# Kernel tuning notes

Measured on AMD Instinct MI355X. Metric: run time of the kernel, lower is better.

The kernel has to match this reference:

```python
import jax, jax.numpy as jnp
import numpy as np

# 3x3 window roll offsets, row-major as in PatchShift2D.shift_content
SHIFTS = [(1, 1), (1, 0), (1, -1), (0, 1), (0, 0), (0, -1), (-1, 1), (-1, 0), (-1, -1)]
NUM_WIN = 9


def patch_shift(x, inv):
    # x: [B, T, H, W, C]; pad C up to multiple of 9 and H,W by 1, roll each
    # of the 9 channel groups by a distinct (h, w) offset, then crop back.
    B, T, H, W, C = x.shape
    Ch = int(np.ceil(C / NUM_WIN) * NUM_WIN)
    xp = jnp.pad(x, ((0, 0), (0, 0), (1, 1), (1, 1), (0, Ch - C)))
    m = -1 if inv else 1
    parts = jnp.split(xp, NUM_WIN, axis=-1)
    shifted = [jnp.roll(p, (m * sh, m * sw), axis=(2, 3))
               for p, (sh, sw) in zip(parts, SHIFTS)]
    return jnp.concatenate(shifted, axis=-1)[:, :, 1:H + 1, 1:W + 1, :C]


def _gelu(v):
    return jax.nn.gelu(v, approximate=False)  # torch nn.GELU default (erf)


def setup_inputs() -> dict:
    key = jax.random.key(0)
    ks = jax.random.split(key, 14)
    B, T, H, W, C = 2, 8, 56, 56, 512
    HID = 1024
    s = 0.02
    return {
        "x": jax.random.normal(ks[0], (B, T, H, W, C), dtype=jnp.float32),
        "fc_w": s * jax.random.normal(ks[1], (C, HID), dtype=jnp.float32),
        "fc_b": jnp.zeros((HID,), jnp.float32),
        "fc1_w": s * jax.random.normal(ks[2], (HID, C), dtype=jnp.float32),
        "fc1_b": jnp.zeros((C,), jnp.float32),
        "fc2_w": s * jax.random.normal(ks[3], (HID, C), dtype=jnp.float32),
        "fc2_b": jnp.zeros((C,), jnp.float32),
        "rw1_w": s * jax.random.normal(ks[4], (C, C // 4), dtype=jnp.float32),
        "rw1_b": jnp.zeros((C // 4,), jnp.float32),
        "rw2_w": s * jax.random.normal(ks[5], (C // 4, 2 * C), dtype=jnp.float32),
        "rw2_b": jnp.zeros((2 * C,), jnp.float32),
        "proj_w": s * jax.random.normal(ks[6], (C, C), dtype=jnp.float32),
        "proj_b": jnp.zeros((C,), jnp.float32),
    }


def reference(x, fc_w, fc_b, fc1_w, fc1_b, fc2_w, fc2_b,
              rw1_w, rw1_b, rw2_w, rw2_b, proj_w, proj_b):
    B, T, H, W, C = x.shape
    xh = _gelu(x @ fc_w + fc_b)                                  # [B,T,H,W,HID]
    h = patch_shift(_gelu(patch_shift(xh, False) @ fc1_w + fc1_b), True)  # [B,T,H,W,C]
    w = _gelu(xh @ fc2_w + fc2_b)                                 # [B,T,H,W,C]
    a = (h + w).mean(axis=(1, 2, 3))                              # [B,C]
    a = _gelu(a @ rw1_w + rw1_b) @ rw2_w + rw2_b                  # [B,2C]
    a = jax.nn.softmax(a.reshape(B, C, 2).transpose(2, 0, 1), axis=0)  # [2,B,C]
    a = a[:, :, None, None, None, :]                              # [2,B,1,1,1,C]
    out = h * a[0] + w * a[1]
    return out @ proj_w + proj_b
```

## Files before the change

### kernel.cpp

```cpp
#include <hip/hip_runtime.h>
#include <hip/hip_bf16.h>
#include <stdint.h>


typedef __attribute__((ext_vector_type(8))) short short8;
typedef __attribute__((ext_vector_type(4))) float floatx4;
typedef unsigned int uint;
typedef unsigned short ushort;

#define NTOK   50176
#define HWIMG  3136

__device__ __forceinline__ float gelu_exact(float v) {
    return 0.5f * v * (1.0f + erff(v * 0.70710678118654752440f));
}
__device__ __forceinline__ float gelu_fast(float v) {
    float u = v * (0.7978845608f + 0.0356774081f * v * v);
    return v * __builtin_amdgcn_rcpf(1.0f + __expf(-2.0f * u));
}

__device__ __forceinline__ int shift_h(int g) { return 1 - g / 3; }
__device__ __forceinline__ int shift_w(int g) { return 1 - g % 3; }

typedef const __attribute__((address_space(1))) uint* gas_ptr;
typedef __attribute__((address_space(3))) uint* las_ptr;

__device__ __forceinline__ void async_copy16(const void* g, void* l) {
    gas_ptr gp = (gas_ptr)(uintptr_t)g;
    las_ptr lp = (las_ptr)(uint32_t)(uintptr_t)l;
    __builtin_amdgcn_global_load_lds(gp, lp, 16, 0, 0);
}

template <int EPI, bool SHIFTA>
__global__ __launch_bounds__(256) void gemm_bt(
    const __hip_bfloat16* __restrict__ A,
    const __hip_bfloat16* __restrict__ Bt,
    const float* __restrict__ bias,
    void* __restrict__ Cout,
    float* __restrict__ ssum, int N, int K)
{
    constexpr int NBUF = SHIFTA ? 1 : 2;
    __shared__ __align__(16) __hip_bfloat16 As[NBUF * 128 * 32];
    __shared__ __align__(16) __hip_bfloat16 Bs[NBUF * 128 * 32];

    const int t    = threadIdx.x;
    const int lane = t & 63;
    const int wave = t >> 6;
    const int wm   = wave >> 1;
    const int wn   = wave & 1;

    const int nbn  = gridDim.x;
    const int flat = blockIdx.y * nbn + blockIdx.x;
    const int xcd  = flat & 7;
    const int j    = flat >> 3;
    const int jd   = j / nbn;
    const int bm   = xcd * 49 + jd;
    const int bn   = j - jd * nbn;

    const int ar0 = bm * 128 + (t >> 2);
    const int ar1 = ar0 + 64;
    const int ac  = (t & 3) * 8;

    const __hip_bfloat16* ga0 = A  + (size_t)ar0 * K + ac;
    const __hip_bfloat16* ga1 = ga0 + (size_t)64 * K;
    const __hip_bfloat16* gb0 = Bt + (size_t)(bn * 128 + (t >> 2)) * K + ac;
    const __hip_bfloat16* gb1 = gb0 + (size_t)64 * K;

    floatx4 acc[4][4] = {};

    const int kq = (lane >> 4) * 8;
    const int ml = lane & 15;

    if constexpr (!SHIFTA) {
        auto stage = [&](int buf) {
            __hip_bfloat16* lA = &As[buf * 4096 + t * 8];
            __hip_bfloat16* lB = &Bs[buf * 4096 + t * 8];
            async_copy16(ga0, lA);
            async_copy16(ga1, lA + 2048);
            async_copy16(gb0, lB);
            async_copy16(gb1, lB + 2048);
            ga0 += 32; ga1 += 32; gb0 += 32; gb1 += 32;
        };

        const int nt = K >> 5;
        stage(0);
        for (int tt = 0; tt < nt; ++tt) {
            const int cur = tt & 1;
            if (tt + 1 < nt) {
                stage(cur ^ 1);
                asm volatile("s_waitcnt vmcnt(4)" ::: "memory");
            } else {
                asm volatile("s_waitcnt vmcnt(0)" ::: "memory");
            }
            __builtin_amdgcn_s_barrier();
            asm volatile("" ::: "memory");

            const int ab = cur * 4096;
            short8 af[4], bf[4];
#pragma unroll
            for (int i = 0; i < 4; i++) {
                af[i] = *(const short8*)&As[ab + (wm * 64 + i * 16 + ml) * 32 + kq];
                bf[i] = *(const short8*)&Bs[ab + (wn * 64 + i * 16 + ml) * 32 + kq];
            }
#pragma unroll
            for (int mi = 0; mi < 4; mi++)
#pragma unroll
                for (int ni = 0; ni < 4; ni++)
                    acc[mi][ni] = __builtin_amdgcn_mfma_f32_16x16x32_bf16(
                        af[mi], bf[ni], acc[mi][ni], 0, 0, 0);

            asm volatile("" ::: "memory");
            __builtin_amdgcn_s_barrier();
        }
    } else {
        __hip_bfloat16* la0 = &As[t * 8];
        __hip_bfloat16* la1 = &As[t * 8 + 2048];
        __hip_bfloat16* lb0 = &Bs[t * 8];
        __hip_bfloat16* lb1 = &Bs[t * 8 + 2048];

        const int rem0 = ar0 % HWIMG, rem1 = ar1 % HWIMG;
        const int oh0 = rem0 / 56, ow0 = rem0 - oh0 * 56;
        const int oh1 = rem1 / 56, ow1 = rem1 - oh1 * 56;

        for (int k0 = 0; k0 < K; k0 += 32) {
            async_copy16(gb0, lb0);
            async_copy16(gb1, lb1);
            gb0 += 32; gb1 += 32;

            uint4 av0 = {0, 0, 0, 0}, av1 = {0, 0, 0, 0};
            {
                const int c0 = k0 + ac;
                const int g  = c0 / 114;
                const int ge = (c0 + 7) / 114;
                if (g == ge) {
                    const int sh = shift_h(g), sw = shift_w(g);
                    const int off = sh * 56 + sw;
                    if ((unsigned)(oh0 - sh) < 56u && (unsigned)(ow0 - sw) < 56u)
                        av0 = *(const uint4*)(A + (size_t)(ar0 - off) * K + c0);
                    if ((unsigned)(oh1 - sh) < 56u && (unsigned)(ow1 - sw) < 56u)
                        av1 = *(const uint4*)(A + (size_t)(ar1 - off) * K + c0);
                } else {
                    union { ushort us[8]; uint4 v; } p0, p1;
#pragma unroll
                    for (int e = 0; e < 8; e++) {
                        const int c  = c0 + e;
                        const int gg = c / 114;
                        const int sh = shift_h(gg), sw = shift_w(gg);
                        const int off = sh * 56 + sw;
                        ushort v0 = 0, v1 = 0;
                        if ((unsigned)(oh0 - sh) < 56u && (unsigned)(ow0 - sw) < 56u)
                            v0 = *(const ushort*)(A + (size_t)(ar0 - off) * K + c);
                        if ((unsigned)(oh1 - sh) < 56u && (unsigned)(ow1 - sw) < 56u)
                            v1 = *(const ushort*)(A + (size_t)(ar1 - off) * K + c);
                        p0.us[e] = v0; p1.us[e] = v1;
                    }
                    av0 = p0.v; av1 = p1.v;
                }
            }

            asm volatile("s_waitcnt vmcnt(0)" ::: "memory");
            *(uint4*)la0 = av0;
            *(uint4*)la1 = av1;
            __syncthreads();

            short8 af[4], bf[4];
#pragma unroll
            for (int i = 0; i < 4; i++) {
                af[i] = *(const short8*)&As[(wm * 64 + i * 16 + ml) * 32 + kq];
                bf[i] = *(const short8*)&Bs[(wn * 64 + i * 16 + ml) * 32 + kq];
            }
#pragma unroll
            for (int mi = 0; mi < 4; mi++)
#pragma unroll
                for (int ni = 0; ni < 4; ni++)
                    acc[mi][ni] = __builtin_amdgcn_mfma_f32_16x16x32_bf16(
                        af[mi], bf[ni], acc[mi][ni], 0, 0, 0);
            __syncthreads();
        }
    }

    const int rq = (lane >> 4) * 4;

    int cols[4], gsh[4], gsw[4];
    float bv[4];
    float sum[4] = {0.f, 0.f, 0.f, 0.f};
#pragma unroll
    for (int ni = 0; ni < 4; ni++) {
        const int col = bn * 128 + wn * 64 + ni * 16 + ml;
        cols[ni] = col;
        bv[ni] = bias[col];
        if (EPI == 2) { const int g = col / 57; gsh[ni] = shift_h(g); gsw[ni] = shift_w(g); }
    }

#pragma unroll
    for (int mi = 0; mi < 4; mi++) {
        const int row0 = bm * 128 + wm * 64 + mi * 16 + rq;
        int phr[4], pwr[4];
        if (EPI == 2) {
            const int bt_ = row0 / HWIMG;
            const int rem = row0 - bt_ * HWIMG;
            const int ph0 = rem / 56;
            const int pw0 = rem - ph0 * 56;
#pragma unroll
            for (int r = 0; r < 4; r++) {
                int pw = pw0 + r, ph = ph0;
                if (pw >= 56) { pw -= 56; ph += 1; }
                if (ph >= 56) { ph = 0; }
                phr[r] = ph; pwr[r] = pw;
            }
        }
#pragma unroll
        for (int ni = 0; ni < 4; ni++) {
            const int col = cols[ni];
#pragma unroll
            for (int r = 0; r < 4; r++) {
                const int tok = row0 + r;
                float v = acc[mi][ni][r] + bv[ni];
                if (EPI != 0) v = gelu_fast(v);
                if (EPI == 0) {
                    ((float*)Cout)[(size_t)tok * N + col] = v;
                } else if (EPI == 1) {
                    ((__hip_bfloat16*)Cout)[(size_t)tok * N + col] = __float2bfloat16(v);
                } else if (EPI == 2) {
                    const int th = phr[r] - gsh[ni], tw = pwr[r] - gsw[ni];
                    if ((unsigned)th < 56u && (unsigned)tw < 56u) {
                        ((__hip_bfloat16*)Cout)[(size_t)(tok - gsh[ni] * 56 - gsw[ni]) * N + col]
                            = __float2bfloat16(v);
                        sum[ni] += v;
                    }
                } else {
                    ((__hip_bfloat16*)Cout)[(size_t)tok * N + col] = __float2bfloat16(v);
                    sum[ni] += v;
                }
            }
        }
    }

    if (EPI == 2 || EPI == 3) {
        const int b = (bm >= 196) ? 1 : 0;
#pragma unroll
        for (int ni = 0; ni < 4; ni++) {
            float s = sum[ni];
            s += __shfl_xor(s, 16, 64);
            s += __shfl_xor(s, 32, 64);
            if (lane < 16) atomicAdd(&ssum[b * 512 + cols[ni]], s);
        }
    }
}

template <int C, int GS, int SGN>
__global__ __launch_bounds__(256) void zero_holes(__hip_bfloat16* __restrict__ buf)
{
    const int i = blockIdx.x * 256 + threadIdx.x;
    const int c = i % C;
    const int p = i / C;
    const int bt = p / 220, fp = p % 220;
    int oh, ow;
    if (fp < 56)       { oh = 0;        ow = fp; }
    else if (fp < 112) { oh = 55;       ow = fp - 56; }
    else if (fp < 166) { oh = fp - 111; ow = 0; }
    else               { oh = fp - 165; ow = 55; }
    const int g = c / GS;
    const int ih = oh - SGN * shift_h(g);
    const int iw = ow - SGN * shift_w(g);
    if ((unsigned)ih >= 56u || (unsigned)iw >= 56u)
        buf[((size_t)(bt * HWIMG + oh * 56 + ow)) * C + c] = __float2bfloat16(0.0f);
}

__global__ __launch_bounds__(256) void cvt_x(const float4* __restrict__ x,
                                             __hip_bfloat16* __restrict__ xb)
{
    int i = blockIdx.x * 256 + threadIdx.x;
    float4 v = x[i];
    __hip_bfloat16 b0 = __float2bfloat16(v.x);
    __hip_bfloat16 b1 = __float2bfloat16(v.y);
    __hip_bfloat16 b2 = __float2bfloat16(v.z);
    __hip_bfloat16 b3 = __float2bfloat16(v.w);
    uint2 o;
    o.x = (uint)*(ushort*)&b0 | ((uint)*(ushort*)&b1 << 16);
    o.y = (uint)*(ushort*)&b2 | ((uint)*(ushort*)&b3 << 16);
    *(uint2*)&xb[(size_t)i * 4] = o;
}

__global__ __launch_bounds__(256) void prep_w(
    const float* __restrict__ fcw,  const float* __restrict__ fc1w,
    const float* __restrict__ fc2w, const float* __restrict__ projw,
    __hip_bfloat16* __restrict__ fcwT, __hip_bfloat16* __restrict__ fc1T,
    __hip_bfloat16* __restrict__ fc2T, __hip_bfloat16* __restrict__ projT)
{
    int i = blockIdx.x * 256 + threadIdx.x;
    if (i < 524288) {
        int n = i >> 9, k = i & 511;
        fcwT[i] = __float2bfloat16(fcw[k * 1024 + n]);
    } else if (i < 1048576) {
        int j = i - 524288;
        int n = j >> 10, k = j & 1023;
        fc1T[j] = __float2bfloat16(fc1w[k * 512 + n]);
    } else if (i < 1572864) {
        int j = i - 1048576;
        int n = j >> 10, k = j & 1023;
        fc2T[j] = __float2bfloat16(fc2w[k * 512 + n]);
    } else if (i < 1835008) {
        int j = i - 1572864;
        int n = j >> 9, k = j & 511;
        projT[j] = __float2bfloat16(projw[k * 512 + n]);
    }
}

__global__ __launch_bounds__(256) void tiny_mlp(
    const float* __restrict__ s0, const float* __restrict__ s1,
    const float* __restrict__ rw1_w, const float* __restrict__ rw1_b,
    const float* __restrict__ rw2_w, const float* __restrict__ rw2_b,
    float* __restrict__ a0, float* __restrict__ a1)
{
    __shared__ float mean[1024];
    __shared__ float z[256];
    __shared__ float av[2048];
    const int t = threadIdx.x;
    for (int i = t; i < 1024; i += 256)
        mean[i] = (s0[i] + s1[i]) * (1.0f / 25088.0f);
    __syncthreads();
    {
        const int b = t >> 7, j = t & 127;
        float acc = rw1_b[j];
        for (int cc = 0; cc < 512; cc++)
            acc += mean[b * 512 + cc] * rw1_w[cc * 128 + j];
        z[t] = gelu_exact(acc);
    }
    __syncthreads();
    for (int i = t; i < 2048; i += 256) {
        const int b = i >> 10, o = i & 1023;
        float acc = rw2_b[o];
        for (int j = 0; j < 128; j++)
            acc += z[b * 128 + j] * rw2_w[j * 1024 + o];
        av[i] = acc;
    }
    __syncthreads();
    for (int i = t; i < 1024; i += 256) {
        const int b = i >> 9, cc = i & 511;
        const float x0 = av[b * 1024 + 2 * cc];
        const float x1 = av[b * 1024 + 2 * cc + 1];
        const float m = fmaxf(x0, x1);
        const float e0 = expf(x0 - m), e1 = expf(x1 - m);
        const float inv = 1.0f / (e0 + e1);
        a0[i] = e0 * inv;
        a1[i] = e1 * inv;
    }
}

__device__ __forceinline__ float bf_lo(uint u) { return __uint_as_float(u << 16); }
__device__ __forceinline__ float bf_hi(uint u) { return __uint_as_float(u & 0xffff0000u); }
__device__ __forceinline__ uint pack_bf2(float lo, float hi) {
    __hip_bfloat16 a = __float2bfloat16(lo), b = __float2bfloat16(hi);
    return (uint)*(ushort*)&a | ((uint)*(ushort*)&b << 16);
}

__global__ __launch_bounds__(256) void combine(
    const uint4* __restrict__ hs4, const uint4* __restrict__ w4,
    const float* __restrict__ a0, const float* __restrict__ a1,
    uint4* __restrict__ hw4)
{
    const int i = blockIdx.x * 256 + threadIdx.x;
    const int ck = i & 63;
    const int tok = i >> 6;
    const int b = (tok >= 25088) ? 1 : 0;
    const float4* A0 = (const float4*)&a0[b * 512 + ck * 8];
    const float4* A1 = (const float4*)&a1[b * 512 + ck * 8];
    const float4 s0l = A0[0], s0h = A0[1];
    const float4 s1l = A1[0], s1h = A1[1];
    const uint4 h = hs4[i], w = w4[i];
    uint4 o;
    o.x = pack_bf2(bf_lo(h.x) * s0l.x + bf_lo(w.x) * s1l.x,
                   bf_hi(h.x) * s0l.y + bf_hi(w.x) * s1l.y);
    o.y = pack_bf2(bf_lo(h.y) * s0l.z + bf_lo(w.y) * s1l.z,
                   bf_hi(h.y) * s0l.w + bf_hi(w.y) * s1l.w);
    o.z = pack_bf2(bf_lo(h.z) * s0h.x + bf_lo(w.z) * s1h.x,
                   bf_hi(h.z) * s0h.y + bf_hi(w.z) * s1h.y);
    o.w = pack_bf2(bf_lo(h.w) * s0h.z + bf_lo(w.w) * s1h.z,
                   bf_hi(h.w) * s0h.w + bf_hi(w.w) * s1h.w);
    hw4[i] = o;
}

extern "C" void kernel_launch(void* const* d_in, const int* in_sizes, int n_in,
                              void* d_out, int out_size, void* d_ws, size_t ws_size,
                              hipStream_t stream)
{
    const float* x      = (const float*)d_in[0];
    const float* fc_w   = (const float*)d_in[1];
    const float* fc_b   = (const float*)d_in[2];
    const float* fc1_w  = (const float*)d_in[3];
    const float* fc1_b  = (const float*)d_in[4];
    const float* fc2_w  = (const float*)d_in[5];
    const float* fc2_b  = (const float*)d_in[6];
    const float* rw1_w  = (const float*)d_in[7];
    const float* rw1_b  = (const float*)d_in[8];
    const float* rw2_w  = (const float*)d_in[9];
    const float* rw2_b  = (const float*)d_in[10];
    const float* proj_w = (const float*)d_in[11];
    const float* proj_b = (const float*)d_in[12];

    uint8_t* ws = (uint8_t*)d_ws;
    __hip_bfloat16* xh  = (__hip_bfloat16*)(ws);
    __hip_bfloat16* xb  = (__hip_bfloat16*)(ws + 102760448);
    uint8_t* wt         = ws + 102760448 + 51380224;
    __hip_bfloat16* fcwT  = (__hip_bfloat16*)(wt);
    __hip_bfloat16* fc1T  = fcwT + 524288;
    __hip_bfloat16* fc2T  = fc1T + 524288;
    __hip_bfloat16* projT = fc2T + 524288;
    float* s0 = (float*)(wt + 3670016);
    float* s1 = s0 + 1024;
    float* a0 = s1 + 1024;
    float* a1 = a0 + 1024;

    __hip_bfloat16* wbuf = (__hip_bfloat16*)d_out;
    __hip_bfloat16* hs   = xb;
    __hip_bfloat16* hw   = xh;

    hipMemsetAsync(s0, 0, 8192, stream);

    cvt_x<<<25088, 256, 0, stream>>>((const float4*)x, xb);
    prep_w<<<7168, 256, 0, stream>>>(fc_w, fc1_w, fc2_w, proj_w, fcwT, fc1T, fc2T, projT);

    gemm_bt<1, false><<<dim3(8, 392), 256, 0, stream>>>(xb, fcwT, fc_b, xh, nullptr, 1024, 512);
    zero_holes<512, 57, -1><<<7040, 256, 0, stream>>>(hs);
    gemm_bt<2, true><<<dim3(4, 392), 256, 0, stream>>>(xh, fc1T, fc1_b, hs, s0, 512, 1024);
    gemm_bt<3, false><<<dim3(4, 392), 256, 0, stream>>>(xh, fc2T, fc2_b, wbuf, s1, 512, 1024);
    tiny_mlp<<<1, 256, 0, stream>>>(s0, s1, rw1_w, rw1_b, rw2_w, rw2_b, a0, a1);
    combine<<<12544, 256, 0, stream>>>((const uint4*)hs, (const uint4*)wbuf, a0, a1, (uint4*)hw);
    gemm_bt<0, false><<<dim3(4, 392), 256, 0, stream>>>(hw, projT, proj_b, d_out, nullptr, 512, 512);
}
```

Baseline: 575.0 us.

## Double-buffer shifted-A GEMM with register prefetch and branchless masked gather

The patch-shift GEMM path now double-buffers its LDS tiles. The next K-tile's shifted A rows are prefetched into registers and its B tile is issued asynchronously while the current tile is computed, so global load latency overlaps the MFMA work. The common single-group case becomes a branchless load with a mask applied afterwards instead of a conditional load. This doubles LDS use for this variant and raises register pressure. The vmcnt(4) wait count must match the number of outstanding loads for the code to stay correct.

Result: slower. 607.3 us (+5.6%).

```diff
diff --git a/kernel.cpp b/kernel.cpp
--- a/kernel.cpp
+++ b/kernel.cpp
@@ -39,9 +39,8 @@
     void* __restrict__ Cout,
     float* __restrict__ ssum, int N, int K)
 {
-    constexpr int NBUF = SHIFTA ? 1 : 2;
-    __shared__ __align__(16) __hip_bfloat16 As[NBUF * 128 * 32];
-    __shared__ __align__(16) __hip_bfloat16 Bs[NBUF * 128 * 32];
+    __shared__ __align__(16) __hip_bfloat16 As[2 * 128 * 32];
+    __shared__ __align__(16) __hip_bfloat16 Bs[2 * 128 * 32];
 
     const int t    = threadIdx.x;
     const int lane = t & 63;
@@ -113,61 +112,76 @@
             __builtin_amdgcn_s_barrier();
         }
     } else {
-        __hip_bfloat16* la0 = &As[t * 8];
-        __hip_bfloat16* la1 = &As[t * 8 + 2048];
-        __hip_bfloat16* lb0 = &Bs[t * 8];
-        __hip_bfloat16* lb1 = &Bs[t * 8 + 2048];
-
         const int rem0 = ar0 % HWIMG, rem1 = ar1 % HWIMG;
         const int oh0 = rem0 / 56, ow0 = rem0 - oh0 * 56;
         const int oh1 = rem1 / 56, ow1 = rem1 - oh1 * 56;
 
-        for (int k0 = 0; k0 < K; k0 += 32) {
-            async_copy16(gb0, lb0);
-            async_copy16(gb1, lb1);
+        auto gather = [&](int k0, uint4& o0, uint4& o1) {
+            const int c0 = k0 + ac;
+            const int gl = c0 / 114;
+            const int gh = (c0 + 7) / 114;
+            const int shl = shift_h(gl), swl = shift_w(gl);
+            const int offl = shl * 56 + swl;
+            const bool v0 = ((unsigned)(oh0 - shl) < 56u) & ((unsigned)(ow0 - swl) < 56u);
+            const bool v1 = ((unsigned)(oh1 - shl) < 56u) & ((unsigned)(ow1 - swl) < 56u);
+            const uint4 l0 = *(const uint4*)(A + (size_t)(ar0 - (v0 ? offl : 0)) * K + c0);
+            const uint4 l1 = *(const uint4*)(A + (size_t)(ar1 - (v1 ? offl : 0)) * K + c0);
+            const uint m0 = v0 ? 0xffffffffu : 0u;
+            const uint m1 = v1 ? 0xffffffffu : 0u;
+            o0.x = l0.x & m0; o0.y = l0.y & m0; o0.z = l0.z & m0; o0.w = l0.w & m0;
+            o1.x = l1.x & m1; o1.y = l1.y & m1; o1.z = l1.z & m1; o1.w = l1.w & m1;
+            if (gl != gh) {
+                union { ushort us[8]; uint4 v; } p0, p1;
+#pragma unroll
+                for (int e = 0; e < 8; e++) {
+                    const int c  = c0 + e;
+                    const int gg = c / 114;
+                    const int sh = shift_h(gg), sw = shift_w(gg);
+                    const int off = sh * 56 + sw;
+                    ushort a0v = 0, a1v = 0;
+                    if ((unsigned)(oh0 - sh) < 56u && (unsigned)(ow0 - sw) < 56u)
+                        a0v = *(const ushort*)(A + (size_t)(ar0 - off) * K + c);
+                    if ((unsigned)(oh1 - sh) < 56u && (unsigned)(ow1 - sw) < 56u)
+                        a1v = *(const ushort*)(A + (size_t)(ar1 - off) * K + c);
+                    p0.us[e] = a0v; p1.us[e] = a1v;
+                }
+                o0 = p0.v; o1 = p1.v;
+            }
+        };
+        auto stageB = [&](int buf) {
+            __hip_bfloat16* lB = &Bs[buf * 4096 + t * 8];
+            async_copy16(gb0, lB);
+            async_copy16(gb1, lB + 2048);
             gb0 += 32; gb1 += 32;
-
-            uint4 av0 = {0, 0, 0, 0}, av1 = {0, 0, 0, 0};
-            {
-                const int c0 = k0 + ac;
-                const int g  = c0 / 114;
-                const int ge = (c0 + 7) / 114;
-                if (g == ge) {
-                    const int sh = shift_h(g), sw = shift_w(g);
-                    const int off = sh * 56 + sw;
-                    if ((unsigned)(oh0 - sh) < 56u && (unsigned)(ow0 - sw) < 56u)
-                        av0 = *(const uint4*)(A + (size_t)(ar0 - off) * K + c0);
-                    if ((unsigned)(oh1 - sh) < 56u && (unsigned)(ow1 - sw) < 56u)
-                        av1 = *(const uint4*)(A + (size_t)(ar1 - off) * K + c0);
-                } else {
-                    union { ushort us[8]; uint4 v; } p0, p1;
-#pragma unroll
-                    for (int e = 0; e < 8; e++) {
-                        const int c  = c0 + e;
-                        const int gg = c / 114;
-                        const int sh = shift_h(gg), sw = shift_w(gg);
-                        const int off = sh * 56 + sw;
-                        ushort v0 = 0, v1 = 0;
-                        if ((unsigned)(oh0 - sh) < 56u && (unsigned)(ow0 - sw) < 56u)
-                            v0 = *(const ushort*)(A + (size_t)(ar0 - off) * K + c);
-                        if ((unsigned)(oh1 - sh) < 56u && (unsigned)(ow1 - sw) < 56u)
-                            v1 = *(const ushort*)(A + (size_t)(ar1 - off) * K + c);
-                        p0.us[e] = v0; p1.us[e] = v1;
-                    }
-                    av0 = p0.v; av1 = p1.v;
-                }
-            }
-
-            asm volatile("s_waitcnt vmcnt(0)" ::: "memory");
-            *(uint4*)la0 = av0;
-            *(uint4*)la1 = av1;
-            __syncthreads();
-
+        };
+
+        const int nt = K >> 5;
+        uint4 pa0, pa1;
+        gather(0, pa0, pa1);
+        stageB(0);
+
+        for (int tt = 0; tt < nt; ++tt) {
+            const int cur = tt & 1;
+            uint4 na0, na1;
+            if (tt + 1 < nt) {
+                gather((tt + 1) * 32, na0, na1);
+                stageB(cur ^ 1);
+            }
+            *(uint4*)&As[cur * 4096 + t * 8]        = pa0;
+            *(uint4*)&As[cur * 4096 + t * 8 + 2048] = pa1;
+            if (tt + 1 < nt)
+                asm volatile("s_waitcnt vmcnt(4) lgkmcnt(0)" ::: "memory");
+            else
+                asm volatile("s_waitcnt vmcnt(0) lgkmcnt(0)" ::: "memory");
+            __builtin_amdgcn_s_barrier();
+            asm volatile("" ::: "memory");
+
+            const int ab = cur * 4096;
             short8 af[4], bf[4];
 #pragma unroll
             for (int i = 0; i < 4; i++) {
-                af[i] = *(const short8*)&As[(wm * 64 + i * 16 + ml) * 32 + kq];
-                bf[i] = *(const short8*)&Bs[(wn * 64 + i * 16 + ml) * 32 + kq];
+                af[i] = *(const short8*)&As[ab + (wm * 64 + i * 16 + ml) * 32 + kq];
+                bf[i] = *(const short8*)&Bs[ab + (wn * 64 + i * 16 + ml) * 32 + kq];
             }
 #pragma unroll
             for (int mi = 0; mi < 4; mi++)
@@ -175,7 +189,10 @@
                 for (int ni = 0; ni < 4; ni++)
                     acc[mi][ni] = __builtin_amdgcn_mfma_f32_16x16x32_bf16(
                         af[mi], bf[ni], acc[mi][ni], 0, 0, 0);
-            __syncthreads();
+
+            asm volatile("" ::: "memory");
+            __builtin_amdgcn_s_barrier();
+            pa0 = na0; pa1 = na1;
         }
     }
 
```
